# Performance work log

Measured on AMD Instinct MI355X. Metric: run time of the kernel, lower is better.

Reference implementation:

```python
import jax, jax.numpy as jnp
import numpy as np

QMAX_W = 127.0   # symmetric int8 for weights
QMAX_A = 255.0   # asymmetric uint8 for activations


def setup_inputs() -> dict:
    key = jax.random.key(0)
    k1, k2, k3 = jax.random.split(key, 3)
    B, S, K, N = 4, 2048, 4096, 4096
    x = jax.random.normal(k1, (B, S, K), dtype=jnp.float32)
    weight = jax.random.normal(k2, (N, K), dtype=jnp.float32) * (1.0 / np.sqrt(K))
    bias = jax.random.normal(k3, (N,), dtype=jnp.float32) * 0.02
    return {"x": x, "weight": weight, "bias": bias}


def reference(x, weight, bias):
    N, K = weight.shape
    # --- weight quantization: row-wise symmetric int8 (absmax / 127) ---
    row_absmax = jnp.max(jnp.abs(weight), axis=1)            # [N]
    row_scales = jnp.where(row_absmax > 0, row_absmax / QMAX_W, 1.0)
    Wq = jnp.clip(jnp.round(weight / row_scales[:, None]), -QMAX_W, QMAX_W)  # int8 values, kept f32 for GEMM

    # --- activation quantization: per-token (column of X^T) asymmetric uint8 ---
    orig_shape = x.shape
    X = x.reshape(-1, K)                                     # [M, K]
    xmin = jnp.min(X, axis=1)                                # [M]
    xmax = jnp.max(X, axis=1)
    rng = xmax - xmin
    col_scales = jnp.where(rng > 0, rng / QMAX_A, 1.0)       # [M]
    col_zps = jnp.round(-xmin / col_scales)                  # [M]
    Xq = jnp.clip(jnp.round(X / col_scales[:, None]) + col_zps[:, None], 0.0, QMAX_A)  # uint8 values

    # --- int GEMM with zero-point correction + dequant: Y[m,n] = s_a[m]*s_w[n]*sum_k (Xq-zp)[m,k]*Wq[n,k] ---
    acc = jnp.einsum('mk,nk->mn', Xq - col_zps[:, None], Wq)  # [M, N]
    Y = acc * (col_scales[:, None] * row_scales[None, :]) + bias
    return Y.reshape(orig_shape[:-1] + (N,))
```

## Files before the change

kernel.cpp:

```cpp
#include <hip/hip_runtime.h>
#include <stdint.h>
#include <stddef.h>

typedef __attribute__((ext_vector_type(4))) int i32x4;

__device__ __forceinline__ void gload_lds16(const void* g, void* l) {
    __builtin_amdgcn_global_load_lds(
        (const __attribute__((address_space(1))) void*)g,
        (__attribute__((address_space(3))) void*)l,
        16, 0, 0);
}

__device__ __forceinline__ float waveAllMaxF(float v) {
#pragma unroll
    for (int m = 32; m > 0; m >>= 1) v = fmaxf(v, __shfl_xor(v, m, 64));
    return v;
}
__device__ __forceinline__ float waveAllMinF(float v) {
#pragma unroll
    for (int m = 32; m > 0; m >>= 1) v = fminf(v, __shfl_xor(v, m, 64));
    return v;
}
__device__ __forceinline__ int waveAllSumI(int v) {
#pragma unroll
    for (int m = 32; m > 0; m >>= 1) v += __shfl_xor(v, m, 64);
    return v;
}

__global__ void __launch_bounds__(256) wquant_kernel(
    const float* __restrict__ W, int8_t* __restrict__ Wq,
    float* __restrict__ rscale, int* __restrict__ rsum, int K) {
    const int n = blockIdx.x * 4 + (threadIdx.x >> 6);
    const int lane = threadIdx.x & 63;
    const float4* row = (const float4*)(W + (size_t)n * K);
    int* out = (int*)(Wq + (size_t)n * K);

    if (K == 4096) {
        float4 v[16];
#pragma unroll
        for (int j = 0; j < 16; ++j) v[j] = row[lane + (j << 6)];

        float amax = 0.f;
#pragma unroll
        for (int j = 0; j < 16; ++j) {
            amax = fmaxf(amax, fmaxf(fmaxf(fabsf(v[j].x), fabsf(v[j].y)),
                                     fmaxf(fabsf(v[j].z), fabsf(v[j].w))));
        }
        amax = waveAllMaxF(amax);
        const float scale = (amax > 0.f) ? (amax / 127.0f) : 1.0f;

        int lsum = 0;
#pragma unroll
        for (int j = 0; j < 16; ++j) {
            int q0 = (int)fminf(fmaxf(rintf(v[j].x / scale), -127.f), 127.f);
            int q1 = (int)fminf(fmaxf(rintf(v[j].y / scale), -127.f), 127.f);
            int q2 = (int)fminf(fmaxf(rintf(v[j].z / scale), -127.f), 127.f);
            int q3 = (int)fminf(fmaxf(rintf(v[j].w / scale), -127.f), 127.f);
            lsum += q0 + q1 + q2 + q3;
            out[lane + (j << 6)] =
                (q0 & 255) | ((q1 & 255) << 8) | ((q2 & 255) << 16) | ((q3 & 255) << 24);
        }
        lsum = waveAllSumI(lsum);
        if (lane == 0) { rsum[n] = lsum; rscale[n] = scale; }
    } else {
        const int K4 = K >> 2;
        float amax = 0.f;
        for (int i = lane; i < K4; i += 64) {
            float4 f = row[i];
            amax = fmaxf(amax, fmaxf(fmaxf(fabsf(f.x), fabsf(f.y)),
                                     fmaxf(fabsf(f.z), fabsf(f.w))));
        }
        amax = waveAllMaxF(amax);
        const float scale = (amax > 0.f) ? (amax / 127.0f) : 1.0f;
        int lsum = 0;
        for (int i = lane; i < K4; i += 64) {
            float4 f = row[i];
            int q0 = (int)fminf(fmaxf(rintf(f.x / scale), -127.f), 127.f);
            int q1 = (int)fminf(fmaxf(rintf(f.y / scale), -127.f), 127.f);
            int q2 = (int)fminf(fmaxf(rintf(f.z / scale), -127.f), 127.f);
            int q3 = (int)fminf(fmaxf(rintf(f.w / scale), -127.f), 127.f);
            lsum += q0 + q1 + q2 + q3;
            out[i] = (q0 & 255) | ((q1 & 255) << 8) | ((q2 & 255) << 16) | ((q3 & 255) << 24);
        }
        lsum = waveAllSumI(lsum);
        if (lane == 0) { rsum[n] = lsum; rscale[n] = scale; }
    }
}

__global__ void __launch_bounds__(256) aquant_kernel(
    const float* __restrict__ X, int8_t* __restrict__ Xq,
    float* __restrict__ cscale, int* __restrict__ azp, int K) {
    const int m = blockIdx.x * 4 + (threadIdx.x >> 6);
    const int lane = threadIdx.x & 63;
    const float4* row = (const float4*)(X + (size_t)m * K);
    int* out = (int*)(Xq + (size_t)m * K);

    if (K == 4096) {
        float4 v[16];
#pragma unroll
        for (int j = 0; j < 16; ++j) v[j] = row[lane + (j << 6)];

        float vmin = 3.402823466e38f, vmax = -3.402823466e38f;
#pragma unroll
        for (int j = 0; j < 16; ++j) {
            vmin = fminf(vmin, fminf(fminf(v[j].x, v[j].y), fminf(v[j].z, v[j].w)));
            vmax = fmaxf(vmax, fmaxf(fmaxf(v[j].x, v[j].y), fmaxf(v[j].z, v[j].w)));
        }
        vmin = waveAllMinF(vmin);
        vmax = waveAllMaxF(vmax);

        const float rng = vmax - vmin;
        const float scale = (rng > 0.f) ? (rng / 255.0f) : 1.0f;
        const float zp = rintf(-vmin / scale);

#pragma unroll
        for (int j = 0; j < 16; ++j) {
            int q0 = (int)fminf(fmaxf(rintf(v[j].x / scale) + zp, 0.f), 255.f) - 128;
            int q1 = (int)fminf(fmaxf(rintf(v[j].y / scale) + zp, 0.f), 255.f) - 128;
            int q2 = (int)fminf(fmaxf(rintf(v[j].z / scale) + zp, 0.f), 255.f) - 128;
            int q3 = (int)fminf(fmaxf(rintf(v[j].w / scale) + zp, 0.f), 255.f) - 128;
            out[lane + (j << 6)] =
                (q0 & 255) | ((q1 & 255) << 8) | ((q2 & 255) << 16) | ((q3 & 255) << 24);
        }
        if (lane == 0) { cscale[m] = scale; azp[m] = 128 - (int)zp; }
    } else {
        const int K4 = K >> 2;
        float vmin = 3.402823466e38f, vmax = -3.402823466e38f;
        for (int i = lane; i < K4; i += 64) {
            float4 f = row[i];
            vmin = fminf(vmin, fminf(fminf(f.x, f.y), fminf(f.z, f.w)));
            vmax = fmaxf(vmax, fmaxf(fmaxf(f.x, f.y), fmaxf(f.z, f.w)));
        }
        vmin = waveAllMinF(vmin);
        vmax = waveAllMaxF(vmax);
        const float rng = vmax - vmin;
        const float scale = (rng > 0.f) ? (rng / 255.0f) : 1.0f;
        const float zp = rintf(-vmin / scale);
        for (int i = lane; i < K4; i += 64) {
            float4 f = row[i];
            int q0 = (int)fminf(fmaxf(rintf(f.x / scale) + zp, 0.f), 255.f) - 128;
            int q1 = (int)fminf(fmaxf(rintf(f.y / scale) + zp, 0.f), 255.f) - 128;
            int q2 = (int)fminf(fmaxf(rintf(f.z / scale) + zp, 0.f), 255.f) - 128;
            int q3 = (int)fminf(fmaxf(rintf(f.w / scale) + zp, 0.f), 255.f) - 128;
            out[i] = (q0 & 255) | ((q1 & 255) << 8) | ((q2 & 255) << 16) | ((q3 & 255) << 24);
        }
        if (lane == 0) { cscale[m] = scale; azp[m] = 128 - (int)zp; }
    }
}

__global__ void __launch_bounds__(512, 2) gemm_i8_kernel(
    const int8_t* __restrict__ A, const int8_t* __restrict__ B,
    float* __restrict__ Y,
    const float* __restrict__ cs, const int* __restrict__ azp,
    const float* __restrict__ rs, const int* __restrict__ rsum,
    const float* __restrict__ bias, int M, int N, int K) {
    extern __shared__ int8_t smem[];

    const int tid = threadIdx.x;
    const int lane = tid & 63;
    const int wave = tid >> 6;
    const int wm = wave >> 2;
    const int wn = wave & 3;
    const int quad = lane >> 4;
    const int lr = lane & 15;

    const int nwg = gridDim.x * gridDim.y;
    int wid = blockIdx.y * gridDim.x + blockIdx.x;
    if ((nwg & 7) == 0) wid = (wid & 7) * (nwg >> 3) + (wid >> 3);
    const int bm = (wid % gridDim.x) * 256;
    const int bn = (wid / gridDim.x) * 256;

    const int8_t* Ag = A + (size_t)bm * K;
    const int8_t* Bg = B + (size_t)bn * K;

    const int sr = tid >> 3;
    const int sc = tid & 7;
    const int csrc = (sc ^ (sr & 7)) << 4;

    i32x4 acc[8][4] = {};

    const int NT = K >> 7;

    {
        int8_t* dA = smem;
        int8_t* dB = smem + 32768;
#pragma unroll
        for (int q = 0; q < 4; ++q) {
            const int r = q * 64 + sr;
            gload_lds16(Ag + (size_t)r * K + csrc, dA + r * 128 + (sc << 4));
            gload_lds16(Bg + (size_t)r * K + csrc, dB + r * 128 + (sc << 4));
        }
    }
    __syncthreads();

    int buf = 0;
    for (int t = 0; t < NT; ++t) {
        if (t + 1 < NT) {
            const int k0 = (t + 1) << 7;
            int8_t* dA = smem + (buf ^ 1) * 65536;
            int8_t* dB = dA + 32768;
#pragma unroll
            for (int q = 0; q < 4; ++q) {
                const int r = q * 64 + sr;
                gload_lds16(Ag + (size_t)r * K + (k0 + csrc), dA + r * 128 + (sc << 4));
                gload_lds16(Bg + (size_t)r * K + (k0 + csrc), dB + r * 128 + (sc << 4));
            }
        }

        const int8_t* Ab = smem + buf * 65536;
        const int8_t* Bb = Ab + 32768;
        const int axor = lr & 7;
#pragma unroll
        for (int kk = 0; kk < 2; ++kk) {
            i32x4 af[8], bf[4];
#pragma unroll
            for (int i = 0; i < 8; ++i) {
                const int row = wm * 128 + i * 16 + lr;
                const int slot = ((kk << 2) | quad) ^ axor;
                af[i] = *(const i32x4*)&Ab[row * 128 + (slot << 4)];
            }
#pragma unroll
            for (int j = 0; j < 4; ++j) {
                const int row = wn * 64 + j * 16 + lr;
                const int slot = ((kk << 2) | quad) ^ axor;
                bf[j] = *(const i32x4*)&Bb[row * 128 + (slot << 4)];
            }
#pragma unroll
            for (int i = 0; i < 8; ++i)
#pragma unroll
                for (int j = 0; j < 4; ++j)
                    acc[i][j] = __builtin_amdgcn_mfma_i32_16x16x64_i8(af[i], bf[j], acc[i][j], 0, 0, 0);
        }

        __syncthreads();
        buf ^= 1;
    }

#pragma unroll
    for (int i = 0; i < 8; ++i) {
        const int mb = bm + wm * 128 + i * 16 + quad * 4;
#pragma unroll
        for (int r = 0; r < 4; ++r) {
            const int m = mb + r;
            const float csm = cs[m];
            const int az = azp[m];
            float* yrow = Y + (size_t)m * N;
#pragma unroll
            for (int j = 0; j < 4; ++j) {
                const int n = bn + wn * 64 + j * 16 + lr;
                const int tot = acc[i][j][r] + az * rsum[n];
                yrow[n] = fmaf((float)tot, csm * rs[n], bias[n]);
            }
        }
    }
}

extern "C" void kernel_launch(void* const* d_in, const int* in_sizes, int n_in,
                              void* d_out, int out_size, void* d_ws, size_t ws_size,
                              hipStream_t stream) {
    const float* x = (const float*)d_in[0];
    const float* w = (const float*)d_in[1];
    const float* bias = (const float*)d_in[2];
    float* y = (float*)d_out;

    const int N = in_sizes[2];
    const int K = in_sizes[1] / N;
    const int M = in_sizes[0] / K;

    uint8_t* ws = (uint8_t*)d_ws;
    int8_t* Wq = (int8_t*)ws;
    int8_t* Xq = (int8_t*)(ws + (size_t)N * K);
    uint8_t* p = ws + (size_t)N * K + (size_t)M * K;
    p = (uint8_t*)(((uintptr_t)p + 255) & ~(uintptr_t)255);
    float* rscale = (float*)p;  p += (size_t)N * sizeof(float);
    int*   rsum   = (int*)p;    p += (size_t)N * sizeof(int);
    float* cscale = (float*)p;  p += (size_t)M * sizeof(float);
    int*   azp    = (int*)p;    p += (size_t)M * sizeof(int);

    static int lds_cfg = 0;
    if (!lds_cfg) {
        (void)hipFuncSetAttribute((const void*)gemm_i8_kernel,
                                  hipFuncAttributeMaxDynamicSharedMemorySize, 131072);
        lds_cfg = 1;
    }

    wquant_kernel<<<N / 4, 256, 0, stream>>>(w, Wq, rscale, rsum, K);
    aquant_kernel<<<M / 4, 256, 0, stream>>>(x, Xq, cscale, azp, K);

    dim3 grid(M / 256, N / 256);
    gemm_i8_kernel<<<grid, 512, 131072, stream>>>(Xq, Wq, y, cscale, azp,
                                                  rscale, rsum, bias, M, N, K);
}
```

Baseline: 407.5 us.

## Interleave prefetch stages with MFMA sub-blocks using fine-grained waitcnt and priority

Splits each K-tile iteration into four phases, each loading one LDS fragment group, issuing part of the next tile's global-to-LDS prefetch, then running a 4x4 MFMA block. Manual vmcnt/lgkmcnt waits and s_barriers replace the single syncthreads, so partially arrived tiles can be consumed earlier. s_setprio raises wave priority during MFMA bursts. Holding only four A fragments at a time lowers register pressure. The cost is many more barriers per iteration and fragile hand-counted waitcnt ordering that must match the order the loads were issued.

New measurement: 405.8 us. Within noise of the previous version (-0.4%).

```diff
diff --git a/kernel.cpp b/kernel.cpp
--- a/kernel.cpp
+++ b/kernel.cpp
@@ -177,64 +177,115 @@
     const int sc = tid & 7;
     const int csrc = (sc ^ (sr & 7)) << 4;
 
+#define STAGE_A(dst, k0, s) { const int r_ = ((s) << 6) + sr; \
+    gload_lds16(Ag + (size_t)r_ * K + ((k0) + csrc), (dst) + r_ * 128 + (sc << 4)); }
+#define STAGE_B(dst, k0, s) { const int r_ = ((s) << 6) + sr; \
+    gload_lds16(Bg + (size_t)r_ * K + ((k0) + csrc), (dst) + 32768 + r_ * 128 + (sc << 4)); }
+
     i32x4 acc[8][4] = {};
-
     const int NT = K >> 7;
 
     {
-        int8_t* dA = smem;
-        int8_t* dB = smem + 32768;
-#pragma unroll
-        for (int q = 0; q < 4; ++q) {
-            const int r = q * 64 + sr;
-            gload_lds16(Ag + (size_t)r * K + csrc, dA + r * 128 + (sc << 4));
-            gload_lds16(Bg + (size_t)r * K + csrc, dB + r * 128 + (sc << 4));
-        }
-    }
-    __syncthreads();
-
-    int buf = 0;
+        int8_t* d = smem;
+        STAGE_B(d, 0, 0) STAGE_B(d, 0, 1) STAGE_B(d, 0, 2) STAGE_B(d, 0, 3)
+        STAGE_A(d, 0, 0) STAGE_A(d, 0, 2) STAGE_A(d, 0, 1) STAGE_A(d, 0, 3)
+    }
+    asm volatile("s_waitcnt vmcnt(2)" ::: "memory");
+    __builtin_amdgcn_sched_barrier(0);
+    __builtin_amdgcn_s_barrier();
+
+    const int axor = lr & 7;
+    const int off_k0 = ((quad ^ axor) << 4);
+    const int off_k1 = (((4 | quad) ^ axor) << 4);
+    const int aBase = (wm * 128 + lr) * 128;
+    const int bBase = (wn * 64 + lr) * 128;
+
     for (int t = 0; t < NT; ++t) {
-        if (t + 1 < NT) {
-            const int k0 = (t + 1) << 7;
-            int8_t* dA = smem + (buf ^ 1) * 65536;
-            int8_t* dB = dA + 32768;
-#pragma unroll
-            for (int q = 0; q < 4; ++q) {
-                const int r = q * 64 + sr;
-                gload_lds16(Ag + (size_t)r * K + (k0 + csrc), dA + r * 128 + (sc << 4));
-                gload_lds16(Bg + (size_t)r * K + (k0 + csrc), dB + r * 128 + (sc << 4));
-            }
-        }
-
-        const int8_t* Ab = smem + buf * 65536;
+        const int8_t* Ab = smem + ((t & 1) << 16);
         const int8_t* Bb = Ab + 32768;
-        const int axor = lr & 7;
-#pragma unroll
-        for (int kk = 0; kk < 2; ++kk) {
-            i32x4 af[8], bf[4];
-#pragma unroll
-            for (int i = 0; i < 8; ++i) {
-                const int row = wm * 128 + i * 16 + lr;
-                const int slot = ((kk << 2) | quad) ^ axor;
-                af[i] = *(const i32x4*)&Ab[row * 128 + (slot << 4)];
-            }
-#pragma unroll
-            for (int j = 0; j < 4; ++j) {
-                const int row = wn * 64 + j * 16 + lr;
-                const int slot = ((kk << 2) | quad) ^ axor;
-                bf[j] = *(const i32x4*)&Bb[row * 128 + (slot << 4)];
-            }
-#pragma unroll
-            for (int i = 0; i < 8; ++i)
-#pragma unroll
-                for (int j = 0; j < 4; ++j)
-                    acc[i][j] = __builtin_amdgcn_mfma_i32_16x16x64_i8(af[i], bf[j], acc[i][j], 0, 0, 0);
-        }
-
-        __syncthreads();
-        buf ^= 1;
-    }
+        int8_t* nb = smem + (((t + 1) & 1) << 16);
+        const int k0n = (t + 1) << 7;
+        const bool pf = (t + 1) < NT;
+
+        i32x4 af[4], bf0[4], bf1[4];
+
+#pragma unroll
+        for (int j = 0; j < 4; ++j) bf0[j] = *(const i32x4*)&Bb[bBase + j * 2048 + off_k0];
+#pragma unroll
+        for (int i = 0; i < 4; ++i) af[i] = *(const i32x4*)&Ab[aBase + i * 2048 + off_k0];
+        if (pf) { STAGE_B(nb, k0n, 0) STAGE_B(nb, k0n, 1) }
+        __builtin_amdgcn_sched_barrier(0);
+        __builtin_amdgcn_s_barrier();
+        asm volatile("s_waitcnt lgkmcnt(0)" ::: "memory");
+        __builtin_amdgcn_sched_barrier(0);
+        __builtin_amdgcn_s_setprio(1);
+#pragma unroll
+        for (int i = 0; i < 4; ++i)
+#pragma unroll
+            for (int j = 0; j < 4; ++j)
+                acc[i][j] = __builtin_amdgcn_mfma_i32_16x16x64_i8(af[i], bf0[j], acc[i][j], 0, 0, 0);
+        __builtin_amdgcn_s_setprio(0);
+        __builtin_amdgcn_sched_barrier(0);
+        __builtin_amdgcn_s_barrier();
+
+#pragma unroll
+        for (int j = 0; j < 4; ++j) bf1[j] = *(const i32x4*)&Bb[bBase + j * 2048 + off_k1];
+#pragma unroll
+        for (int i = 0; i < 4; ++i) af[i] = *(const i32x4*)&Ab[aBase + i * 2048 + off_k1];
+        if (pf) { STAGE_B(nb, k0n, 2) STAGE_B(nb, k0n, 3) }
+        __builtin_amdgcn_sched_barrier(0);
+        __builtin_amdgcn_s_barrier();
+        asm volatile("s_waitcnt lgkmcnt(0)" ::: "memory");
+        __builtin_amdgcn_sched_barrier(0);
+        __builtin_amdgcn_s_setprio(1);
+#pragma unroll
+        for (int i = 0; i < 4; ++i)
+#pragma unroll
+            for (int j = 0; j < 4; ++j)
+                acc[i][j] = __builtin_amdgcn_mfma_i32_16x16x64_i8(af[i], bf1[j], acc[i][j], 0, 0, 0);
+        __builtin_amdgcn_s_setprio(0);
+        __builtin_amdgcn_sched_barrier(0);
+        if (pf) { asm volatile("s_waitcnt vmcnt(4)" ::: "memory"); }
+        else    { asm volatile("s_waitcnt vmcnt(0)" ::: "memory"); }
+        __builtin_amdgcn_s_barrier();
+
+#pragma unroll
+        for (int i = 0; i < 4; ++i) af[i] = *(const i32x4*)&Ab[aBase + 8192 + i * 2048 + off_k0];
+        if (pf) { STAGE_A(nb, k0n, 0) STAGE_A(nb, k0n, 2) }
+        __builtin_amdgcn_sched_barrier(0);
+        __builtin_amdgcn_s_barrier();
+        asm volatile("s_waitcnt lgkmcnt(0)" ::: "memory");
+        __builtin_amdgcn_sched_barrier(0);
+        __builtin_amdgcn_s_setprio(1);
+#pragma unroll
+        for (int i = 0; i < 4; ++i)
+#pragma unroll
+            for (int j = 0; j < 4; ++j)
+                acc[4 + i][j] = __builtin_amdgcn_mfma_i32_16x16x64_i8(af[i], bf0[j], acc[4 + i][j], 0, 0, 0);
+        __builtin_amdgcn_s_setprio(0);
+        __builtin_amdgcn_sched_barrier(0);
+        __builtin_amdgcn_s_barrier();
+
+#pragma unroll
+        for (int i = 0; i < 4; ++i) af[i] = *(const i32x4*)&Ab[aBase + 8192 + i * 2048 + off_k1];
+        if (pf) { STAGE_A(nb, k0n, 1) STAGE_A(nb, k0n, 3) }
+        __builtin_amdgcn_sched_barrier(0);
+        __builtin_amdgcn_s_barrier();
+        asm volatile("s_waitcnt lgkmcnt(0)" ::: "memory");
+        __builtin_amdgcn_sched_barrier(0);
+        __builtin_amdgcn_s_setprio(1);
+#pragma unroll
+        for (int i = 0; i < 4; ++i)
+#pragma unroll
+            for (int j = 0; j < 4; ++j)
+                acc[4 + i][j] = __builtin_amdgcn_mfma_i32_16x16x64_i8(af[i], bf1[j], acc[4 + i][j], 0, 0, 0);
+        __builtin_amdgcn_s_setprio(0);
+        __builtin_amdgcn_sched_barrier(0);
+        if (pf) { asm volatile("s_waitcnt vmcnt(2)" ::: "memory"); }
+        __builtin_amdgcn_s_barrier();
+    }
+#undef STAGE_A
+#undef STAGE_B
 
 #pragma unroll
     for (int i = 0; i < 8; ++i) {
```
